# Kernel optimization log

Hardware: AMD Instinct MI355X
Metric: run time of the kernel (lower is better)

Reference implementation:

```python
import jax, jax.numpy as jnp
import numpy as np

HIDDEN = 1024
HEADS = 16
N, T1, T2 = 2, 2048, 2048


def setup_inputs() -> dict:
    key = jax.random.key(0)
    k1, k2, k3, k4 = jax.random.split(key, 4)
    q = jax.random.normal(k1, (N, T1, HIDDEN), dtype=jnp.float32)
    encoder_k = jax.random.normal(k2, (N, T2, HIDDEN), dtype=jnp.float32)
    encoder_v = jax.random.normal(k3, (N, T2, HIDDEN), dtype=jnp.float32)
    encoder_attention_mask = jnp.zeros((N, 1, T2, T2), dtype=jnp.float32)
    wo_w = jax.random.normal(k4, (HIDDEN, HIDDEN), dtype=jnp.float32) * (1.0 / np.sqrt(HIDDEN))
    wo_b = jnp.zeros((HIDDEN,), dtype=jnp.float32)
    return {"q": q, "encoder_k": encoder_k, "encoder_v": encoder_v,
            "encoder_attention_mask": encoder_attention_mask,
            "wo_w": wo_w, "wo_b": wo_b}


def _split_heads(x):
    # [N, T, E] -> [N, h, T, d]
    n, t, e = x.shape
    return x.reshape(n, t, HEADS, e // HEADS).transpose(0, 2, 1, 3)


def reference(q, encoder_k, encoder_v, encoder_attention_mask, wo_w, wo_b):
    qh = _split_heads(q)            # [N,h,T1,d]
    kh = _split_heads(encoder_k)    # [N,h,T2,d]
    vh = _split_heads(encoder_v)    # [N,h,T2,d]
    # NOTE: original applies no 1/sqrt(d) scaling
    scores = jnp.einsum('bhqd,bhkd->bhqk', qh, kh) + encoder_attention_mask
    weights = jax.nn.softmax(scores, axis=-1)
    ctx = jnp.einsum('bhqk,bhkd->bhqd', weights, vh)   # [N,h,T1,d]
    ctx = ctx.transpose(0, 2, 1, 3).reshape(q.shape[0], q.shape[1], -1)  # [N,T1,E]
    # wo: Linear (torch: x @ W.T + b) followed by ReLU
    return jax.nn.relu(ctx @ wo_w.T + wo_b)
```

## Files before the change

### kernel.cpp

```cpp
#include <hip/hip_runtime.h>


typedef short short8 __attribute__((ext_vector_type(8)));
typedef short short4v __attribute__((ext_vector_type(4)));
typedef float floatx4 __attribute__((ext_vector_type(4)));

#define HIDDEN 1024
#define HEADS 16
#define NB 2
#define T1 2048
#define T2 2048

#define LOG2E 1.44269504f
#define SHIFT 28.8539004f
#define VS 72

__device__ __forceinline__ float fexp2(float x) {
#if __has_builtin(__builtin_amdgcn_exp2f)
    return __builtin_amdgcn_exp2f(x);
#else
    return __expf(x * 0.69314718056f);
#endif
}

__device__ __forceinline__ unsigned short f2bf(float f) {
    unsigned u = __float_as_uint(f);
    return (unsigned short)((u + 0x7fffu + ((u >> 16) & 1u)) >> 16);
}

__device__ __forceinline__ int pk_hi16(float a, float b) {
    return (int)__builtin_amdgcn_perm(__float_as_uint(b), __float_as_uint(a), 0x07060302u);
}

union S4 { int2 i2; short4v s; };

__global__ void zero_kernel(unsigned* f) {
    if (threadIdx.x == 0) *f = 0u;
}

__global__ __launch_bounds__(256) void prep_kernel(
        const float4* __restrict__ ek, const float4* __restrict__ ev,
        const float4* __restrict__ ww, const float4* __restrict__ mask,
        ushort4* __restrict__ Khm,
        ushort4* __restrict__ Wb,
        short*   __restrict__ Vt,
        unsigned* __restrict__ flag)
{
    __shared__ short lds[64 * 68];
    const int t = threadIdx.x;
    if (blockIdx.y == 0) {
        const int NKf4 = NB * T2 * HIDDEN / 4;
        const int n = NKf4 + HIDDEN * HIDDEN / 4;
        int i = blockIdx.x * 256 + t;
        const int stride = gridDim.x * 256;
        for (; i < n; i += stride) {
            if (i < NKf4) {
                float4 v = ek[i];
                ushort4 o;
                o.x = f2bf(v.x); o.y = f2bf(v.y); o.z = f2bf(v.z); o.w = f2bf(v.w);
                int b = i >> 19, r = i & 524287;
                int key = r >> 8, c4 = r & 255;
                int h = c4 >> 4, d4 = c4 & 15;
                Khm[(((b * 16 + h) * 2048 + key) << 4) + d4] = o;
            } else {
                float4 v = ww[i - NKf4];
                ushort4 o;
                o.x = f2bf(v.x); o.y = f2bf(v.y); o.z = f2bf(v.z); o.w = f2bf(v.w);
                Wb[i - NKf4] = o;
            }
        }
    } else if (blockIdx.y == 1) {
        const int NM = NB * T2 * T2 / 4;
        int i = blockIdx.x * 256 + t;
        const int stride = gridDim.x * 256;
        float mx = 0.f;
        for (; i < NM; i += stride) {
            float4 v = mask[i];
            mx = fmaxf(mx, fmaxf(fmaxf(fabsf(v.x), fabsf(v.y)), fmaxf(fabsf(v.z), fabsf(v.w))));
        }
        for (int d = 32; d; d >>= 1) mx = fmaxf(mx, __shfl_xor(mx, d));
        if ((t & 63) == 0 && mx > 0.f) atomicMax(flag, __float_as_uint(mx));
    } else {
        const int x = blockIdx.x;
        const int kt = x & 31, h = (x >> 5) & 15, b = x >> 9;
        const int key0 = kt * 64;
#pragma unroll
        for (int it = 0; it < 4; ++it) {
            int idx = t + it * 256;
            int key = idx >> 4, f4 = idx & 15;
            float4 v = ev[(b * T2 + key0 + key) * 256 + h * 16 + f4];
            short4v o;
            o[0] = (short)f2bf(v.x); o[1] = (short)f2bf(v.y);
            o[2] = (short)f2bf(v.z); o[3] = (short)f2bf(v.w);
            *(short4v*)&lds[key * 68 + f4 * 4] = o;
        }
        __syncthreads();
        const int dim = t >> 2, kq = t & 3;
        short8 s0, s1;
#pragma unroll
        for (int kk = 0; kk < 8; ++kk) s0[kk] = lds[(kq * 16 + kk) * 68 + dim];
#pragma unroll
        for (int kk = 0; kk < 8; ++kk) s1[kk] = lds[(kq * 16 + 8 + kk) * 68 + dim];
        short* Vr = Vt + ((b * 16 + h) * 64 + dim) * T2 + key0 + kq * 16;
        *(short8*)&Vr[0] = s0;
        *(short8*)&Vr[8] = s1;
    }
}

__global__ __launch_bounds__(256) void attn_kernel(
        const float* __restrict__ q,
        const short* __restrict__ Khm,
        const short* __restrict__ Vt,
        const float* __restrict__ mask,
        const unsigned* __restrict__ flagp,
        short* __restrict__ ctx)
{
    __shared__ short lV[2][64 * VS];

    const int tid = threadIdx.x;
    const int wave = tid >> 6;
    const int lane = tid & 63;
    const int quad = lane >> 4;
    const int l16 = lane & 15;

    const int b = blockIdx.z;
    const int h = blockIdx.y;
    const int qrow = blockIdx.x * 64 + wave * 16 + l16;

    const bool use_mask = (*flagp != 0u);

    const short* Kp = Khm + ((b * 16 + h) * 2048) * 64;
    const short* Vp = Vt + ((b * 16 + h) * 64) * 2048;
    const float* mrow = mask + ((long)(b * T2) + qrow) * T2;

    short8 qf[2];
#pragma unroll
    for (int ks = 0; ks < 2; ++ks) {
        const float* qp = q + (((b * T1) + qrow) << 10) + (h << 6) + ks * 32 + quad * 8;
        float4 v0 = *(const float4*)qp;
        float4 v1 = *(const float4*)(qp + 4);
        short8 s;
        s[0] = (short)f2bf(v0.x * LOG2E); s[1] = (short)f2bf(v0.y * LOG2E);
        s[2] = (short)f2bf(v0.z * LOG2E); s[3] = (short)f2bf(v0.w * LOG2E);
        s[4] = (short)f2bf(v1.x * LOG2E); s[5] = (short)f2bf(v1.y * LOG2E);
        s[6] = (short)f2bf(v1.z * LOG2E); s[7] = (short)f2bf(v1.w * LOG2E);
        qf[ks] = s;
    }

    floatx4 o_acc[4], o_l;
#pragma unroll
    for (int cb = 0; cb < 4; ++cb) o_acc[cb] = (floatx4){0.f, 0.f, 0.f, 0.f};
    o_l = (floatx4){0.f, 0.f, 0.f, 0.f};
    short4v ones;
#pragma unroll
    for (int j = 0; j < 4; ++j) ones[j] = (short)0x3F80;

#pragma unroll
    for (int it = 0; it < 2; ++it) {
        int c = tid + it * 256;
        int dim = c >> 3, kb8 = c & 7;
        *(short8*)&lV[0][dim * VS + kb8 * 8] = *(const short8*)&Vp[dim * 2048 + kb8 * 8];
    }
    __syncthreads();

    for (int ic = 0; ic < T2 / 64; ++ic) {
        const int kc = ic << 6;
        const short* cur = lV[ic & 1];
        if (ic + 1 < T2 / 64) {
            short* nxt = lV[(ic + 1) & 1];
#pragma unroll
            for (int it = 0; it < 2; ++it) {
                int c = tid + it * 256;
                int dim = c >> 3, kb8 = c & 7;
                *(short8*)&nxt[dim * VS + kb8 * 8] =
                    *(const short8*)&Vp[dim * 2048 + kc + 64 + kb8 * 8];
            }
        }

        short8 kf[4][2];
#pragma unroll
        for (int kb = 0; kb < 4; ++kb)
#pragma unroll
            for (int ks = 0; ks < 2; ++ks)
                kf[kb][ks] = *(const short8*)&Kp[(kc + kb * 16 + l16) * 64 + ks * 32 + quad * 8];

        short4v vf[4][4];
#pragma unroll
        for (int kb = 0; kb < 4; ++kb)
#pragma unroll
            for (int cb = 0; cb < 4; ++cb)
                vf[kb][cb] = *(const short4v*)&cur[(cb * 16 + l16) * VS + kb * 16 + quad * 4];

        floatx4 st[4];
#pragma unroll
        for (int kb = 0; kb < 4; ++kb) {
            floatx4 a = (floatx4){-SHIFT, -SHIFT, -SHIFT, -SHIFT};
            a = __builtin_amdgcn_mfma_f32_16x16x32_bf16(kf[kb][0], qf[0], a, 0, 0, 0);
            a = __builtin_amdgcn_mfma_f32_16x16x32_bf16(kf[kb][1], qf[1], a, 0, 0, 0);
            st[kb] = a;
        }
        if (use_mask) {
#pragma unroll
            for (int kb = 0; kb < 4; ++kb)
#pragma unroll
                for (int r = 0; r < 4; ++r)
                    st[kb][r] += mrow[kc + kb * 16 + quad * 4 + r] * LOG2E;
        }
        short4v pf[4];
#pragma unroll
        for (int kb = 0; kb < 4; ++kb) {
            float p0 = fexp2(st[kb][0]);
            float p1 = fexp2(st[kb][1]);
            float p2 = fexp2(st[kb][2]);
            float p3 = fexp2(st[kb][3]);
            S4 u; u.i2 = make_int2(pk_hi16(p0, p1), pk_hi16(p2, p3));
            pf[kb] = u.s;
        }
#pragma unroll
        for (int kb = 0; kb < 4; ++kb) {
            o_l = __builtin_amdgcn_mfma_f32_16x16x16bf16_1k(ones, pf[kb], o_l, 0, 0, 0);
#pragma unroll
            for (int cb = 0; cb < 4; ++cb)
                o_acc[cb] = __builtin_amdgcn_mfma_f32_16x16x16bf16_1k(
                    vf[kb][cb], pf[kb], o_acc[cb], 0, 0, 0);
        }
        __syncthreads();
    }

    const float rinv = 1.0f / o_l[0];
#pragma unroll
    for (int cb = 0; cb < 4; ++cb) {
        short4v o;
#pragma unroll
        for (int r = 0; r < 4; ++r) o[r] = (short)f2bf(o_acc[cb][r] * rinv);
        *(short4v*)&ctx[((b * T1 + qrow) << 10) + (h << 6) + cb * 16 + quad * 4] = o;
    }
}

__global__ __launch_bounds__(256) void proj_kernel(
        const short* __restrict__ Cb,
        const short* __restrict__ Wb,
        const float* __restrict__ bias,
        float* __restrict__ out)
{
    __shared__ short lA[128 * 72];
    __shared__ short lB[128 * 72];

    const int tid = threadIdx.x;
    const int wave = tid >> 6;
    const int lane = tid & 63;
    const int quad = lane >> 4;
    const int l16 = lane & 15;
    const int wm = wave >> 1, wn = wave & 1;
    const int bm = blockIdx.x, bn = blockIdx.y;

    floatx4 acc[4][4];
#pragma unroll
    for (int i = 0; i < 4; ++i)
#pragma unroll
        for (int j = 0; j < 4; ++j) acc[i][j] = (floatx4){0.f, 0.f, 0.f, 0.f};

    for (int kt = 0; kt < 1024; kt += 64) {
#pragma unroll
        for (int it = 0; it < 4; ++it) {
            int i = tid + it * 256;
            int row = i >> 3, c = i & 7;
            *(short8*)&lA[row * 72 + c * 8] =
                *(const short8*)&Cb[((bm * 128 + row) << 10) + kt + c * 8];
            *(short8*)&lB[row * 72 + c * 8] =
                *(const short8*)&Wb[((bn * 128 + row) << 10) + kt + c * 8];
        }
        __syncthreads();
#pragma unroll
        for (int ks = 0; ks < 2; ++ks) {
            short8 af[4], bf[4];
#pragma unroll
            for (int i = 0; i < 4; ++i) {
                af[i] = *(const short8*)&lA[(wm * 64 + i * 16 + l16) * 72 + ks * 32 + quad * 8];
                bf[i] = *(const short8*)&lB[(wn * 64 + i * 16 + l16) * 72 + ks * 32 + quad * 8];
            }
#pragma unroll
            for (int i = 0; i < 4; ++i)
#pragma unroll
                for (int j = 0; j < 4; ++j)
                    acc[i][j] = __builtin_amdgcn_mfma_f32_16x16x32_bf16(af[i], bf[j], acc[i][j], 0, 0, 0);
        }
        __syncthreads();
    }

    float bv[4];
#pragma unroll
    for (int j = 0; j < 4; ++j) bv[j] = bias[bn * 128 + wn * 64 + j * 16 + l16];

#pragma unroll
    for (int i = 0; i < 4; ++i)
#pragma unroll
        for (int j = 0; j < 4; ++j)
#pragma unroll
            for (int r = 0; r < 4; ++r) {
                int row = bm * 128 + wm * 64 + i * 16 + quad * 4 + r;
                int col = bn * 128 + wn * 64 + j * 16 + l16;
                float v = acc[i][j][r] + bv[j];
                out[(row << 10) + col] = fmaxf(v, 0.f);
            }
}

extern "C" void kernel_launch(void* const* d_in, const int* in_sizes, int n_in,
                              void* d_out, int out_size, void* d_ws, size_t ws_size,
                              hipStream_t stream) {
    const float* q    = (const float*)d_in[0];
    const float* ek   = (const float*)d_in[1];
    const float* ev   = (const float*)d_in[2];
    const float* mask = (const float*)d_in[3];
    const float* wo_w = (const float*)d_in[4];
    const float* wo_b = (const float*)d_in[5];
    float* out = (float*)d_out;

    char* ws = (char*)d_ws;
    unsigned* flag = (unsigned*)ws;
    short* Khm = (short*)(ws + 4096);
    short* Wb  = Khm + (NB * T2 * HIDDEN);
    short* Vt  = Wb + (HIDDEN * HIDDEN);
    short* Cb  = Vt + (NB * T2 * HIDDEN);

    zero_kernel<<<1, 64, 0, stream>>>(flag);
    prep_kernel<<<dim3(1024, 3), 256, 0, stream>>>(
        (const float4*)ek, (const float4*)ev, (const float4*)wo_w, (const float4*)mask,
        (ushort4*)Khm, (ushort4*)Wb, Vt, flag);
    attn_kernel<<<dim3(T1 / 64, HEADS, NB), 256, 0, stream>>>(q, Khm, Vt, mask, flag, Cb);
    proj_kernel<<<dim3(32, 8), 256, 0, stream>>>(Cb, Wb, wo_b, out);
}
```

Baseline: 272.1 us.

## Software-pipeline K and V loads across chunks and repad V LDS tile

K fragments for the next chunk are now loaded into registers while the current chunk's QK MFMAs run, instead of being loaded at the start of each iteration. V tiles for the next chunk are read from global memory into registers early and written to LDS after the score MFMAs, so global latency overlaps compute. The LDS row pitch for V changes from 72 to 68 shorts, with stores split into 8-byte halves to keep alignment. V fragment reads move inside the kb loop to cut register pressure. The trade-off is more live registers for prefetched data and possibly different LDS bank conflict patterns.

```diff
diff --git a/kernel.cpp b/kernel.cpp
--- a/kernel.cpp
+++ b/kernel.cpp
@@ -13,7 +13,7 @@
 
 #define LOG2E 1.44269504f
 #define SHIFT 28.8539004f
-#define VS 72
+#define VS 68
 
 __device__ __forceinline__ float fexp2(float x) {
 #if __has_builtin(__builtin_amdgcn_exp2f)
@@ -33,6 +33,7 @@
 }
 
 union S4 { int2 i2; short4v s; };
+union S8 { short8 s8; short4v s4[2]; };
 
 __global__ void zero_kernel(unsigned* f) {
     if (threadIdx.x == 0) *f = 0u;
@@ -133,6 +134,9 @@
     const short* Vp = Vt + ((b * 16 + h) * 64) * 2048;
     const float* mrow = mask + ((long)(b * T2) + qrow) * T2;
 
+    const int sdim = tid >> 3, sk8 = tid & 7;
+    const int sdim2 = (tid + 256) >> 3;
+
     short8 qf[2];
 #pragma unroll
     for (int ks = 0; ks < 2; ++ks) {
@@ -155,41 +159,34 @@
 #pragma unroll
     for (int j = 0; j < 4; ++j) ones[j] = (short)0x3F80;
 
-#pragma unroll
-    for (int it = 0; it < 2; ++it) {
-        int c = tid + it * 256;
-        int dim = c >> 3, kb8 = c & 7;
-        *(short8*)&lV[0][dim * VS + kb8 * 8] = *(const short8*)&Vp[dim * 2048 + kb8 * 8];
-    }
+    {
+        S8 v0, v1;
+        v0.s8 = *(const short8*)&Vp[sdim * 2048 + sk8 * 8];
+        v1.s8 = *(const short8*)&Vp[sdim2 * 2048 + sk8 * 8];
+        *(short4v*)&lV[0][sdim * VS + sk8 * 8] = v0.s4[0];
+        *(short4v*)&lV[0][sdim * VS + sk8 * 8 + 4] = v0.s4[1];
+        *(short4v*)&lV[0][sdim2 * VS + sk8 * 8] = v1.s4[0];
+        *(short4v*)&lV[0][sdim2 * VS + sk8 * 8 + 4] = v1.s4[1];
+    }
+    short8 kf[4][2];
+#pragma unroll
+    for (int kb = 0; kb < 4; ++kb)
+#pragma unroll
+        for (int ks = 0; ks < 2; ++ks)
+            kf[kb][ks] = *(const short8*)&Kp[(kb * 16 + l16) * 64 + ks * 32 + quad * 8];
     __syncthreads();
 
-    for (int ic = 0; ic < T2 / 64; ++ic) {
+    const int NC = T2 / 64;
+    for (int ic = 0; ic < NC; ++ic) {
         const int kc = ic << 6;
         const short* cur = lV[ic & 1];
-        if (ic + 1 < T2 / 64) {
-            short* nxt = lV[(ic + 1) & 1];
-#pragma unroll
-            for (int it = 0; it < 2; ++it) {
-                int c = tid + it * 256;
-                int dim = c >> 3, kb8 = c & 7;
-                *(short8*)&nxt[dim * VS + kb8 * 8] =
-                    *(const short8*)&Vp[dim * 2048 + kc + 64 + kb8 * 8];
-            }
-        }
-
-        short8 kf[4][2];
-#pragma unroll
-        for (int kb = 0; kb < 4; ++kb)
-#pragma unroll
-            for (int ks = 0; ks < 2; ++ks)
-                kf[kb][ks] = *(const short8*)&Kp[(kc + kb * 16 + l16) * 64 + ks * 32 + quad * 8];
-
-        short4v vf[4][4];
-#pragma unroll
-        for (int kb = 0; kb < 4; ++kb)
-#pragma unroll
-            for (int cb = 0; cb < 4; ++cb)
-                vf[kb][cb] = *(const short4v*)&cur[(cb * 16 + l16) * VS + kb * 16 + quad * 4];
+        const bool more = (ic + 1 < NC);
+
+        S8 vt0, vt1;
+        if (more) {
+            vt0.s8 = *(const short8*)&Vp[sdim * 2048 + kc + 64 + sk8 * 8];
+            vt1.s8 = *(const short8*)&Vp[sdim2 * 2048 + kc + 64 + sk8 * 8];
+        }
 
         floatx4 st[4];
 #pragma unroll
@@ -199,6 +196,24 @@
             a = __builtin_amdgcn_mfma_f32_16x16x32_bf16(kf[kb][1], qf[1], a, 0, 0, 0);
             st[kb] = a;
         }
+
+        if (more) {
+#pragma unroll
+            for (int kb = 0; kb < 4; ++kb)
+#pragma unroll
+                for (int ks = 0; ks < 2; ++ks)
+                    kf[kb][ks] = *(const short8*)
+                        &Kp[(kc + 64 + kb * 16 + l16) * 64 + ks * 32 + quad * 8];
+        }
+
+        if (more) {
+            short* nxt = (short*)lV[(ic + 1) & 1];
+            *(short4v*)&nxt[sdim * VS + sk8 * 8] = vt0.s4[0];
+            *(short4v*)&nxt[sdim * VS + sk8 * 8 + 4] = vt0.s4[1];
+            *(short4v*)&nxt[sdim2 * VS + sk8 * 8] = vt1.s4[0];
+            *(short4v*)&nxt[sdim2 * VS + sk8 * 8 + 4] = vt1.s4[1];
+        }
+
         if (use_mask) {
 #pragma unroll
             for (int kb = 0; kb < 4; ++kb)
@@ -216,13 +231,18 @@
             S4 u; u.i2 = make_int2(pk_hi16(p0, p1), pk_hi16(p2, p3));
             pf[kb] = u.s;
         }
+
 #pragma unroll
         for (int kb = 0; kb < 4; ++kb) {
+            short4v vf[4];
+#pragma unroll
+            for (int cb = 0; cb < 4; ++cb)
+                vf[cb] = *(const short4v*)&cur[(cb * 16 + l16) * VS + kb * 16 + quad * 4];
             o_l = __builtin_amdgcn_mfma_f32_16x16x16bf16_1k(ones, pf[kb], o_l, 0, 0, 0);
 #pragma unroll
             for (int cb = 0; cb < 4; ++cb)
                 o_acc[cb] = __builtin_amdgcn_mfma_f32_16x16x16bf16_1k(
-                    vf[kb][cb], pf[kb], o_acc[cb], 0, 0, 0);
+                    vf[cb], pf[kb], o_acc[cb], 0, 0, 0);
         }
         __syncthreads();
     }
```

Result: no change. 273.1 us (+0.3%).

## Split attention over key halves, double query rows per wave, add combine kernel

Applied to the files above, without the earlier changes.

The attention kernel now processes 32 query rows per wave (two 16-row blocks) so each K fragment and staged V tile is reused twice, and it splits the key range into two halves across blockIdx.z. Each half writes unnormalized fp32 partial outputs and row sums, which a new combine kernel adds, normalizes and converts to bf16. K fragments are software-pipelined with double-buffered registers, and the V LDS stride changes to 68. In exchange it adds fp32 partial-output traffic through global memory, an extra kernel launch and higher register pressure.

```diff
diff --git a/kernel.cpp b/kernel.cpp
--- a/kernel.cpp
+++ b/kernel.cpp
@@ -13,7 +13,7 @@
 
 #define LOG2E 1.44269504f
 #define SHIFT 28.8539004f
-#define VS 72
+#define VS 68
 
 __device__ __forceinline__ float fexp2(float x) {
 #if __has_builtin(__builtin_amdgcn_exp2f)
@@ -33,6 +33,7 @@
 }
 
 union S4 { int2 i2; short4v s; };
+union S8 { short8 s8; short4v s4[2]; };
 
 __global__ void zero_kernel(unsigned* f) {
     if (threadIdx.x == 0) *f = 0u;
@@ -107,104 +108,60 @@
     }
 }
 
-__global__ __launch_bounds__(256) void attn_kernel(
-        const float* __restrict__ q,
-        const short* __restrict__ Khm,
-        const short* __restrict__ Vt,
-        const float* __restrict__ mask,
-        const unsigned* __restrict__ flagp,
-        short* __restrict__ ctx)
-{
-    __shared__ short lV[2][64 * VS];
-
-    const int tid = threadIdx.x;
-    const int wave = tid >> 6;
-    const int lane = tid & 63;
-    const int quad = lane >> 4;
-    const int l16 = lane & 15;
-
-    const int b = blockIdx.z;
-    const int h = blockIdx.y;
-    const int qrow = blockIdx.x * 64 + wave * 16 + l16;
-
-    const bool use_mask = (*flagp != 0u);
-
-    const short* Kp = Khm + ((b * 16 + h) * 2048) * 64;
-    const short* Vp = Vt + ((b * 16 + h) * 64) * 2048;
-    const float* mrow = mask + ((long)(b * T2) + qrow) * T2;
-
-    short8 qf[2];
-#pragma unroll
-    for (int ks = 0; ks < 2; ++ks) {
-        const float* qp = q + (((b * T1) + qrow) << 10) + (h << 6) + ks * 32 + quad * 8;
-        float4 v0 = *(const float4*)qp;
-        float4 v1 = *(const float4*)(qp + 4);
-        short8 s;
-        s[0] = (short)f2bf(v0.x * LOG2E); s[1] = (short)f2bf(v0.y * LOG2E);
-        s[2] = (short)f2bf(v0.z * LOG2E); s[3] = (short)f2bf(v0.w * LOG2E);
-        s[4] = (short)f2bf(v1.x * LOG2E); s[5] = (short)f2bf(v1.y * LOG2E);
-        s[6] = (short)f2bf(v1.z * LOG2E); s[7] = (short)f2bf(v1.w * LOG2E);
-        qf[ks] = s;
-    }
-
-    floatx4 o_acc[4], o_l;
-#pragma unroll
-    for (int cb = 0; cb < 4; ++cb) o_acc[cb] = (floatx4){0.f, 0.f, 0.f, 0.f};
-    o_l = (floatx4){0.f, 0.f, 0.f, 0.f};
-    short4v ones;
-#pragma unroll
-    for (int j = 0; j < 4; ++j) ones[j] = (short)0x3F80;
-
+struct KFrag { short8 f[4][2]; };
+
+__device__ __forceinline__ void load_k(KFrag& k, const short* __restrict__ Kp,
+                                       int kc, int l16, int quad) {
+#pragma unroll
+    for (int kb = 0; kb < 4; ++kb)
+#pragma unroll
+        for (int ks = 0; ks < 2; ++ks)
+            k.f[kb][ks] = *(const short8*)&Kp[(kc + kb * 16 + l16) * 64 + ks * 32 + quad * 8];
+}
+
+__device__ __forceinline__ void stage_v(short* __restrict__ buf, const short* __restrict__ Vp,
+                                        int kc, int tid) {
 #pragma unroll
     for (int it = 0; it < 2; ++it) {
-        int c = tid + it * 256;
-        int dim = c >> 3, kb8 = c & 7;
-        *(short8*)&lV[0][dim * VS + kb8 * 8] = *(const short8*)&Vp[dim * 2048 + kb8 * 8];
-    }
-    __syncthreads();
-
-    for (int ic = 0; ic < T2 / 64; ++ic) {
-        const int kc = ic << 6;
-        const short* cur = lV[ic & 1];
-        if (ic + 1 < T2 / 64) {
-            short* nxt = lV[(ic + 1) & 1];
-#pragma unroll
-            for (int it = 0; it < 2; ++it) {
-                int c = tid + it * 256;
-                int dim = c >> 3, kb8 = c & 7;
-                *(short8*)&nxt[dim * VS + kb8 * 8] =
-                    *(const short8*)&Vp[dim * 2048 + kc + 64 + kb8 * 8];
-            }
-        }
-
-        short8 kf[4][2];
-#pragma unroll
-        for (int kb = 0; kb < 4; ++kb)
-#pragma unroll
-            for (int ks = 0; ks < 2; ++ks)
-                kf[kb][ks] = *(const short8*)&Kp[(kc + kb * 16 + l16) * 64 + ks * 32 + quad * 8];
-
-        short4v vf[4][4];
-#pragma unroll
-        for (int kb = 0; kb < 4; ++kb)
-#pragma unroll
-            for (int cb = 0; cb < 4; ++cb)
-                vf[kb][cb] = *(const short4v*)&cur[(cb * 16 + l16) * VS + kb * 16 + quad * 4];
-
+        int idx = tid + (it << 8);
+        int dim = idx >> 3, k8 = idx & 7;
+        S8 v;
+        v.s8 = *(const short8*)&Vp[dim * 2048 + kc + k8 * 8];
+        *(short4v*)&buf[dim * VS + k8 * 8] = v.s4[0];
+        *(short4v*)&buf[dim * VS + k8 * 8 + 4] = v.s4[1];
+    }
+}
+
+__device__ __forceinline__ void do_chunk(
+        const KFrag& kf, const short* __restrict__ cur,
+        const short8 (&qf)[2][2], floatx4 (&o_acc)[2][4], floatx4 (&o_l)[2],
+        const float* __restrict__ mq, int kc, bool use_mask,
+        int quad, int l16, short4v ones)
+{
+    short4v vfrag[4][4];
+#pragma unroll
+    for (int kb = 0; kb < 4; ++kb)
+#pragma unroll
+        for (int cb = 0; cb < 4; ++cb)
+            vfrag[kb][cb] = *(const short4v*)&cur[(cb * 16 + l16) * VS + kb * 16 + quad * 4];
+
+#pragma unroll
+    for (int rb = 0; rb < 2; ++rb) {
         floatx4 st[4];
 #pragma unroll
         for (int kb = 0; kb < 4; ++kb) {
             floatx4 a = (floatx4){-SHIFT, -SHIFT, -SHIFT, -SHIFT};
-            a = __builtin_amdgcn_mfma_f32_16x16x32_bf16(kf[kb][0], qf[0], a, 0, 0, 0);
-            a = __builtin_amdgcn_mfma_f32_16x16x32_bf16(kf[kb][1], qf[1], a, 0, 0, 0);
+            a = __builtin_amdgcn_mfma_f32_16x16x32_bf16(kf.f[kb][0], qf[rb][0], a, 0, 0, 0);
+            a = __builtin_amdgcn_mfma_f32_16x16x32_bf16(kf.f[kb][1], qf[rb][1], a, 0, 0, 0);
             st[kb] = a;
         }
         if (use_mask) {
+            const float* mrow = mq + (long)(rb * 16 + l16) * T2 + kc;
 #pragma unroll
             for (int kb = 0; kb < 4; ++kb)
 #pragma unroll
                 for (int r = 0; r < 4; ++r)
-                    st[kb][r] += mrow[kc + kb * 16 + quad * 4 + r] * LOG2E;
+                    st[kb][r] += mrow[kb * 16 + quad * 4 + r] * LOG2E;
         }
         short4v pf[4];
 #pragma unroll
@@ -218,22 +175,125 @@
         }
 #pragma unroll
         for (int kb = 0; kb < 4; ++kb) {
-            o_l = __builtin_amdgcn_mfma_f32_16x16x16bf16_1k(ones, pf[kb], o_l, 0, 0, 0);
+            o_l[rb] = __builtin_amdgcn_mfma_f32_16x16x16bf16_1k(ones, pf[kb], o_l[rb], 0, 0, 0);
 #pragma unroll
             for (int cb = 0; cb < 4; ++cb)
-                o_acc[cb] = __builtin_amdgcn_mfma_f32_16x16x16bf16_1k(
-                    vf[kb][cb], pf[kb], o_acc[cb], 0, 0, 0);
-        }
-        __syncthreads();
-    }
-
-    const float rinv = 1.0f / o_l[0];
-#pragma unroll
-    for (int cb = 0; cb < 4; ++cb) {
-        short4v o;
-#pragma unroll
-        for (int r = 0; r < 4; ++r) o[r] = (short)f2bf(o_acc[cb][r] * rinv);
-        *(short4v*)&ctx[((b * T1 + qrow) << 10) + (h << 6) + cb * 16 + quad * 4] = o;
+                o_acc[rb][cb] = __builtin_amdgcn_mfma_f32_16x16x16bf16_1k(
+                    vfrag[kb][cb], pf[kb], o_acc[rb][cb], 0, 0, 0);
+        }
+    }
+}
+
+__global__ __launch_bounds__(256) void attn_kernel(
+        const float* __restrict__ q,
+        const short* __restrict__ Khm,
+        const short* __restrict__ Vt,
+        const float* __restrict__ mask,
+        const unsigned* __restrict__ flagp,
+        float* __restrict__ Op,
+        float* __restrict__ Lp)
+{
+    __shared__ short lV[2][64 * VS];
+
+    const int tid = threadIdx.x;
+    const int wave = tid >> 6;
+    const int lane = tid & 63;
+    const int quad = lane >> 4;
+    const int l16 = lane & 15;
+
+    const int b = blockIdx.z >> 1;
+    const int s = blockIdx.z & 1;
+    const int koff = s << 10;
+    const int h = blockIdx.y;
+    const int q0 = blockIdx.x * 128;
+
+    const bool use_mask = (*flagp != 0u);
+
+    const short* Kp = Khm + ((b * 16 + h) * 2048 + koff) * 64;
+    const short* Vp = Vt + ((b * 16 + h) * 64) * 2048 + koff;
+    const float* mq = mask + ((long)(b * T2) + q0 + wave * 32) * T2 + koff;
+
+    short8 qf[2][2];
+#pragma unroll
+    for (int rb = 0; rb < 2; ++rb) {
+#pragma unroll
+        for (int ks = 0; ks < 2; ++ks) {
+            const float* qp = q + (((b * T1) + q0 + wave * 32 + rb * 16 + l16) << 10)
+                                + (h << 6) + ks * 32 + quad * 8;
+            float4 v0 = *(const float4*)qp;
+            float4 v1 = *(const float4*)(qp + 4);
+            short8 sv;
+            sv[0] = (short)f2bf(v0.x * LOG2E); sv[1] = (short)f2bf(v0.y * LOG2E);
+            sv[2] = (short)f2bf(v0.z * LOG2E); sv[3] = (short)f2bf(v0.w * LOG2E);
+            sv[4] = (short)f2bf(v1.x * LOG2E); sv[5] = (short)f2bf(v1.y * LOG2E);
+            sv[6] = (short)f2bf(v1.z * LOG2E); sv[7] = (short)f2bf(v1.w * LOG2E);
+            qf[rb][ks] = sv;
+        }
+    }
+
+    floatx4 o_acc[2][4], o_l[2];
+#pragma unroll
+    for (int rb = 0; rb < 2; ++rb) {
+        o_l[rb] = (floatx4){0.f, 0.f, 0.f, 0.f};
+#pragma unroll
+        for (int cb = 0; cb < 4; ++cb) o_acc[rb][cb] = (floatx4){0.f, 0.f, 0.f, 0.f};
+    }
+    short4v ones;
+#pragma unroll
+    for (int j = 0; j < 4; ++j) ones[j] = (short)0x3F80;
+
+    KFrag kf0, kf1;
+    load_k(kf0, Kp, 0, l16, quad);
+    stage_v(lV[0], Vp, 0, tid);
+    __syncthreads();
+
+    const int NC = 16;
+    for (int ic = 0; ic < NC; ic += 2) {
+        stage_v(lV[1], Vp, (ic + 1) << 6, tid);
+        load_k(kf1, Kp, (ic + 1) << 6, l16, quad);
+        do_chunk(kf0, lV[0], qf, o_acc, o_l, mq, ic << 6, use_mask, quad, l16, ones);
+        __syncthreads();
+        if (ic + 2 < NC) {
+            stage_v(lV[0], Vp, (ic + 2) << 6, tid);
+            load_k(kf0, Kp, (ic + 2) << 6, l16, quad);
+        }
+        do_chunk(kf1, lV[1], qf, o_acc, o_l, mq, (ic + 1) << 6, use_mask, quad, l16, ones);
+        __syncthreads();
+    }
+
+    float* Opb = Op + ((long)(s * NB + b) * T1) * 1024;
+#pragma unroll
+    for (int rb = 0; rb < 2; ++rb) {
+        const int qrow = q0 + wave * 32 + rb * 16 + l16;
+#pragma unroll
+        for (int cb = 0; cb < 4; ++cb)
+            *(floatx4*)&Opb[((long)qrow << 10) + (h << 6) + cb * 16 + quad * 4] = o_acc[rb][cb];
+        if (quad == 0)
+            Lp[(((s * NB + b) * 16 + h) << 11) + qrow] = o_l[rb][0];
+    }
+}
+
+__global__ __launch_bounds__(256) void combine_kernel(
+        const float4* __restrict__ Op,
+        const float* __restrict__ Lp,
+        ushort4* __restrict__ Cb)
+{
+    const int NT = NB * T1 * 256;
+    int i = blockIdx.x * 256 + threadIdx.x;
+    const int stride = gridDim.x * 256;
+    for (; i < NT; i += stride) {
+        int d4 = i & 255, row = (i >> 8) & 2047, b = i >> 19;
+        int h = d4 >> 4;
+        float4 a0 = Op[i];
+        float4 a1 = Op[NT + i];
+        float l = Lp[((b * 16 + h) << 11) + row] + Lp[(((NB + b) * 16 + h) << 11) + row];
+        float rinv = 1.0f / l;
+        ushort4 o;
+        o.x = f2bf((a0.x + a1.x) * rinv);
+        o.y = f2bf((a0.y + a1.y) * rinv);
+        o.z = f2bf((a0.z + a1.z) * rinv);
+        o.w = f2bf((a0.w + a1.w) * rinv);
+        Cb[i] = o;
     }
 }
 
@@ -322,11 +382,15 @@
     short* Wb  = Khm + (NB * T2 * HIDDEN);
     short* Vt  = Wb + (HIDDEN * HIDDEN);
     short* Cb  = Vt + (NB * T2 * HIDDEN);
+    float* Op  = (float*)(Cb + (NB * T1 * HIDDEN));
+    float* Lp  = Op + 2 * NB * T1 * HIDDEN;
 
     zero_kernel<<<1, 64, 0, stream>>>(flag);
     prep_kernel<<<dim3(1024, 3), 256, 0, stream>>>(
         (const float4*)ek, (const float4*)ev, (const float4*)wo_w, (const float4*)mask,
         (ushort4*)Khm, (ushort4*)Wb, Vt, flag);
-    attn_kernel<<<dim3(T1 / 64, HEADS, NB), 256, 0, stream>>>(q, Khm, Vt, mask, flag, Cb);
+    attn_kernel<<<dim3(T1 / 128, HEADS, NB * 2), 256, 0, stream>>>(
+        q, Khm, Vt, mask, flag, Op, Lp);
+    combine_kernel<<<1024, 256, 0, stream>>>((const float4*)Op, Lp, (ushort4*)Cb);
     proj_kernel<<<dim3(32, 8), 256, 0, stream>>>(Cb, Wb, wo_b, out);
 }
```

Result: faster. 252.9 us (-7.1%).
